# Optimization experiments

Measured on AMD Instinct MI355X. Metric: run time of the kernel, lower is better.

## Reference

```python
import jax, jax.numpy as jnp
import numpy as np

TEMPERATURE = 0.1
NUM_CLASSES = 4  # matches fill_max of labels
NEG_INF = -1e9
EPS = 1e-6


def setup_inputs() -> dict:
    key = jax.random.key(0)
    k1, k2 = jax.random.split(key)
    emb = jax.random.normal(k1, (2, 128, 64, 64), dtype=jnp.float32)
    labels = jax.random.randint(k2, (2, 64, 64), 0, NUM_CLASSES, dtype=jnp.int32)
    return {"emb": emb, "labels": labels}


def reference(emb, labels):
    B, C, H, W = emb.shape
    e = emb.transpose(0, 2, 3, 1).reshape(B * H * W, C)      # [N, C]
    lab = labels.reshape(B * H * W)                           # [N]
    # F.normalize(dim=1) with eps clamp
    norm = jnp.maximum(jnp.linalg.norm(e, axis=1, keepdims=True), 1e-12)
    e = e / norm
    n = e.shape[0]
    logits = (e @ e.T) / TEMPERATURE                          # [N, N]
    diag = jnp.arange(n)
    logits = logits.at[diag, diag].set(NEG_INF)               # mask self
    ex = jnp.exp(logits)                                      # [N, N]
    same = lab[:, None] == lab[None, :]                       # [N, N] bool
    pos_sum = jnp.sum(jnp.where(same, ex, 0.0), axis=1)       # [N]
    tot_sum = jnp.sum(ex, axis=1)                             # [N]
    row_loss = -jnp.log(pos_sum / (tot_sum + EPS))            # [N]
    # per-class mean, averaged over classes present (== torch.unique loop)
    sums = jax.ops.segment_sum(row_loss, lab, num_segments=NUM_CLASSES)
    counts = jax.ops.segment_sum(jnp.ones_like(row_loss), lab, num_segments=NUM_CLASSES)
    present = counts > 0
    per_cls = jnp.where(present, sums / jnp.maximum(counts, 1.0), 0.0)
    return per_cls.sum() / present.sum()
```

## Files before the change

kernel.cpp:

```cpp
#include <hip/hip_runtime.h>
#include <hip/hip_bf16.h>

#define N_PIX 8192
#define C_DIM 128
#define HW 4096
#define PRESCALE 3.7982825f
#define NUM_CLASSES 4

typedef __attribute__((ext_vector_type(8))) short short8;
typedef __attribute__((ext_vector_type(4))) float float4v;


__global__ __launch_bounds__(256) void normscale_kernel(const float* __restrict__ emb,
                                                        unsigned short* __restrict__ ebfT,
                                                        float* __restrict__ pz) {
    const int tid = threadIdx.x;
    const int p16 = tid & 15;
    const int g = tid >> 4;
    const int n = blockIdx.x * 16 + p16;
    const int b = n >> 12;
    const int hw = n & (HW - 1);
    const float* base = emb + b * (C_DIM * HW) + hw;

    float v[8];
    float ss = 0.f;
#pragma unroll
    for (int i = 0; i < 8; ++i) {
        v[i] = base[(g * 8 + i) * HW];
        ss += v[i] * v[i];
    }
    ss += __shfl_xor(ss, 16, 64);
    ss += __shfl_xor(ss, 32, 64);
    __shared__ float red[4][16];
    const int wv = tid >> 6;
    if ((tid & 63) < 16) red[wv][p16] = ss;
    __syncthreads();
    float tot = red[0][p16] + red[1][p16] + red[2][p16] + red[3][p16];
    float inv = PRESCALE / fmaxf(sqrtf(tot), 1e-12f);

    unsigned short us[8];
#pragma unroll
    for (int i = 0; i < 8; ++i) {
        __hip_bfloat16 h = __float2bfloat16(v[i] * inv);
        us[i] = *reinterpret_cast<unsigned short*>(&h);
    }
    const int s = g >> 2, quad = g & 3;
    unsigned short* dst = ebfT + (((blockIdx.x * 4 + s) * 64 + quad * 16 + p16) << 3);
    *reinterpret_cast<short8*>(dst) = *reinterpret_cast<short8*>(us);

    if (blockIdx.x < 64) pz[blockIdx.x * 256 + tid] = 0.f;
}

__global__ __launch_bounds__(256, 4) void pairwise_kernel(const unsigned short* __restrict__ ebfT,
                                                          const int* __restrict__ lab,
                                                          float* __restrict__ pos,
                                                          float* __restrict__ tot) {
    const int bi = blockIdx.x;
    const int d = blockIdx.y + 1;
    if (d == 32 && bi >= 32) return;
    const bool diag = (d == 33);
    const int jp = diag ? bi : ((bi + d) & 63);
    const int Ipanel = bi << 7;
    const int Jpanel = jp << 7;

    const int wave = threadIdx.x >> 6;
    const int lane = threadIdx.x & 63;
    const int quad = lane >> 4;
    const int lq = lane & 15;

    const int I0 = Ipanel + wave * 32;

    __shared__ float2 cpart[4][8][64];

    short8 afrag[2][4];
#pragma unroll
    for (int a = 0; a < 2; ++a) {
        const unsigned short* ab = ebfT + ((((I0 >> 4) + a) * 4) * 64 + lane) * 8;
#pragma unroll
        for (int s = 0; s < 4; ++s)
            afrag[a][s] = *reinterpret_cast<const short8*>(ab + s * 512);
    }
    int lab_row[2][4];
#pragma unroll
    for (int a = 0; a < 2; ++a)
#pragma unroll
        for (int r = 0; r < 4; ++r) lab_row[a][r] = lab[I0 + a * 16 + quad * 4 + r];

    float tacc[2][4] = {};
    float pacc[2][4] = {};

    if (!diag) {
        const unsigned short* bbase = ebfT + ((Jpanel >> 4) * 4 * 64 + lane) * 8;
#pragma unroll 2
        for (int t = 0; t < 8; ++t) {
            const int lab_col = lab[Jpanel + t * 16 + lq];
            const unsigned short* bt = bbase + t * 2048;
            short8 bfrag[4];
#pragma unroll
            for (int s = 0; s < 4; ++s)
                bfrag[s] = *reinterpret_cast<const short8*>(bt + s * 512);

            float4v acc0 = {0.f, 0.f, 0.f, 0.f};
            float4v acc1 = {0.f, 0.f, 0.f, 0.f};
#pragma unroll
            for (int s = 0; s < 4; ++s) {
                acc0 = __builtin_amdgcn_mfma_f32_16x16x32_bf16(afrag[0][s], bfrag[s], acc0, 0, 0, 0);
                acc1 = __builtin_amdgcn_mfma_f32_16x16x32_bf16(afrag[1][s], bfrag[s], acc1, 0, 0, 0);
            }

            float colTs = 0.f, colPs = 0.f;
#pragma unroll
            for (int r = 0; r < 4; ++r) {
                float ex = __builtin_amdgcn_exp2f(acc0[r]);
                tacc[0][r] += ex;
                float pxe = (lab_row[0][r] == lab_col) ? ex : 0.f;
                pacc[0][r] += pxe;
                colTs += ex;
                colPs += pxe;
            }
#pragma unroll
            for (int r = 0; r < 4; ++r) {
                float ex = __builtin_amdgcn_exp2f(acc1[r]);
                tacc[1][r] += ex;
                float pxe = (lab_row[1][r] == lab_col) ? ex : 0.f;
                pacc[1][r] += pxe;
                colTs += ex;
                colPs += pxe;
            }
            cpart[wave][t][lane] = make_float2(colTs, colPs);
        }
    } else {
#define EPILOGUE(A, ACC, MASKED)                                            \
    {                                                                       \
        _Pragma("unroll") for (int r = 0; r < 4; ++r) {                     \
            float ex = __builtin_amdgcn_exp2f(ACC[r]);                      \
            if (MASKED) ex = (lq == quad * 4 + r) ? 0.f : ex;               \
            tacc[A][r] += ex;                                               \
            pacc[A][r] += (lab_row[A][r] == lab_col) ? ex : 0.f;            \
        }                                                                   \
    }
        const unsigned short* bbase = ebfT + ((Ipanel >> 4) * 4 * 64 + lane) * 8;
#pragma unroll 2
        for (int t = 0; t < 8; ++t) {
            const int J = Ipanel + t * 16;
            const int lab_col = lab[J + lq];
            const unsigned short* bt = bbase + t * 2048;
            short8 bfrag[4];
#pragma unroll
            for (int s = 0; s < 4; ++s)
                bfrag[s] = *reinterpret_cast<const short8*>(bt + s * 512);

            float4v acc0 = {0.f, 0.f, 0.f, 0.f};
            float4v acc1 = {0.f, 0.f, 0.f, 0.f};
#pragma unroll
            for (int s = 0; s < 4; ++s) {
                acc0 = __builtin_amdgcn_mfma_f32_16x16x32_bf16(afrag[0][s], bfrag[s], acc0, 0, 0, 0);
                acc1 = __builtin_amdgcn_mfma_f32_16x16x32_bf16(afrag[1][s], bfrag[s], acc1, 0, 0, 0);
            }
            if (J == I0) EPILOGUE(0, acc0, true) else EPILOGUE(0, acc0, false);
            if (J == I0 + 16) EPILOGUE(1, acc1, true) else EPILOGUE(1, acc1, false);
        }
#undef EPILOGUE
    }

#pragma unroll
    for (int a = 0; a < 2; ++a) {
#pragma unroll
        for (int r = 0; r < 4; ++r) {
            float t = tacc[a][r], p = pacc[a][r];
#pragma unroll
            for (int off = 1; off < 16; off <<= 1) {
                t += __shfl_xor(t, off, 64);
                p += __shfl_xor(p, off, 64);
            }
            if (lq == 0) {
                const int row = I0 + a * 16 + quad * 4 + r;
                atomicAdd(&tot[row], t);
                atomicAdd(&pos[row], p);
            }
        }
    }

    if (!diag) {
        __syncthreads();
        if (threadIdx.x < 128) {
            const int j = threadIdx.x;
            const int tt = j >> 4, jl = j & 15;
            float st = 0.f, sp = 0.f;
#pragma unroll
            for (int w = 0; w < 4; ++w)
#pragma unroll
                for (int q = 0; q < 4; ++q) {
                    float2 v = cpart[w][tt][q * 16 + jl];
                    st += v.x;
                    sp += v.y;
                }
            atomicAdd(&tot[Jpanel + j], st);
            atomicAdd(&pos[Jpanel + j], sp);
        }
    }
}

__global__ __launch_bounds__(1024) void finalize_kernel(const float* __restrict__ pos,
                                                        const float* __restrict__ tot,
                                                        const int* __restrict__ lab,
                                                        float* __restrict__ out) {
    const int tid = threadIdx.x;
    float tv[8], pv[8];
    int cl[8];
#pragma unroll
    for (int it = 0; it < 8; ++it) {
        const int n = it * 1024 + tid;
        tv[it] = tot[n];
        pv[it] = pos[n];
        cl[it] = lab[n];
    }
    float ls[NUM_CLASSES] = {0.f, 0.f, 0.f, 0.f};
    float lc[NUM_CLASSES] = {0.f, 0.f, 0.f, 0.f};
#pragma unroll
    for (int it = 0; it < 8; ++it) {
        float rl = logf(tv[it] + 1e-6f) - logf(pv[it]);
#pragma unroll
        for (int k = 0; k < NUM_CLASSES; ++k) {
            if (cl[it] == k) {
                ls[k] += rl;
                lc[k] += 1.f;
            }
        }
    }
#pragma unroll
    for (int off = 1; off < 64; off <<= 1) {
#pragma unroll
        for (int k = 0; k < NUM_CLASSES; ++k) {
            ls[k] += __shfl_xor(ls[k], off, 64);
            lc[k] += __shfl_xor(lc[k], off, 64);
        }
    }
    __shared__ float ssum[16][NUM_CLASSES];
    __shared__ float scnt[16][NUM_CLASSES];
    const int wid = tid >> 6;
    if ((tid & 63) == 0) {
#pragma unroll
        for (int k = 0; k < NUM_CLASSES; ++k) {
            ssum[wid][k] = ls[k];
            scnt[wid][k] = lc[k];
        }
    }
    __syncthreads();
    if (tid == 0) {
        float acc = 0.f;
        int present = 0;
        for (int k = 0; k < NUM_CLASSES; ++k) {
            float s = 0.f, c = 0.f;
            for (int w = 0; w < 16; ++w) {
                s += ssum[w][k];
                c += scnt[w][k];
            }
            if (c > 0.f) {
                acc += s / c;
                present++;
            }
        }
        out[0] = acc / (float)(present > 0 ? present : 1);
    }
}

extern "C" void kernel_launch(void* const* d_in, const int* in_sizes, int n_in,
                              void* d_out, int out_size, void* d_ws, size_t ws_size,
                              hipStream_t stream) {
    const float* emb = (const float*)d_in[0];
    const int* lab = (const int*)d_in[1];
    float* out = (float*)d_out;

    unsigned short* ebfT = (unsigned short*)d_ws;
    float* pos = (float*)((char*)d_ws + N_PIX * C_DIM * 2);
    float* tot = pos + N_PIX;

    normscale_kernel<<<N_PIX / 16, 256, 0, stream>>>(emb, ebfT, pos);

    dim3 grid(64, 33);
    pairwise_kernel<<<grid, 256, 0, stream>>>(ebfT, lab, pos, tot);

    finalize_kernel<<<1, 1024, 0, stream>>>(pos, tot, lab, out);
}
```

Before: 88.56 us.

## Replace per-row float atomics with slot-partitioned partial sums and parallel reduce

The pairwise kernel now writes its per-row and per-column partial exp sums into dedicated slots indexed by diagonal offset, instead of doing atomicAdd into shared row accumulators. A new 64-block reduce kernel sums the 64 slots per row, computes row losses, and accumulates per-class sums with atomics. The last block to finish, detected through a counter, writes the final scalar. This removes atomic contention and replaces the single-block finalize. The cost is about 4 MB of extra partial-sum traffic and a slot-mapping scheme that must cover each row exactly once.

```diff
diff --git a/kernel.cpp b/kernel.cpp
--- a/kernel.cpp
+++ b/kernel.cpp
@@ -6,6 +6,7 @@
 #define HW 4096
 #define PRESCALE 3.7982825f
 #define NUM_CLASSES 4
+#define NSLOT 65
 
 typedef __attribute__((ext_vector_type(8))) short short8;
 typedef __attribute__((ext_vector_type(4))) float float4v;
@@ -13,7 +14,7 @@
 
 __global__ __launch_bounds__(256) void normscale_kernel(const float* __restrict__ emb,
                                                         unsigned short* __restrict__ ebfT,
-                                                        float* __restrict__ pz) {
+                                                        unsigned* __restrict__ czero) {
     const int tid = threadIdx.x;
     const int p16 = tid & 15;
     const int g = tid >> 4;
@@ -48,13 +49,13 @@
     unsigned short* dst = ebfT + (((blockIdx.x * 4 + s) * 64 + quad * 16 + p16) << 3);
     *reinterpret_cast<short8*>(dst) = *reinterpret_cast<short8*>(us);
 
-    if (blockIdx.x < 64) pz[blockIdx.x * 256 + tid] = 0.f;
+    if (blockIdx.x == 0 && tid < 9) czero[tid] = 0u;
 }
 
 __global__ __launch_bounds__(256, 4) void pairwise_kernel(const unsigned short* __restrict__ ebfT,
                                                           const int* __restrict__ lab,
-                                                          float* __restrict__ pos,
-                                                          float* __restrict__ tot) {
+                                                          float* __restrict__ tpart,
+                                                          float* __restrict__ ppart) {
     const int bi = blockIdx.x;
     const int d = blockIdx.y + 1;
     if (d == 32 && bi >= 32) return;
@@ -163,20 +164,24 @@
 #undef EPILOGUE
     }
 
-#pragma unroll
-    for (int a = 0; a < 2; ++a) {
-#pragma unroll
-        for (int r = 0; r < 4; ++r) {
-            float t = tacc[a][r], p = pacc[a][r];
-#pragma unroll
-            for (int off = 1; off < 16; off <<= 1) {
-                t += __shfl_xor(t, off, 64);
-                p += __shfl_xor(p, off, 64);
-            }
-            if (lq == 0) {
-                const int row = I0 + a * 16 + quad * 4 + r;
-                atomicAdd(&tot[row], t);
-                atomicAdd(&pos[row], p);
+    {
+        float* trow = tpart + (d - 1) * N_PIX;
+        float* prow = ppart + (d - 1) * N_PIX;
+#pragma unroll
+        for (int a = 0; a < 2; ++a) {
+#pragma unroll
+            for (int r = 0; r < 4; ++r) {
+                float t = tacc[a][r], p = pacc[a][r];
+#pragma unroll
+                for (int off = 1; off < 16; off <<= 1) {
+                    t += __shfl_xor(t, off, 64);
+                    p += __shfl_xor(p, off, 64);
+                }
+                if (lq == 0) {
+                    const int row = I0 + a * 16 + quad * 4 + r;
+                    trow[row] = t;
+                    prow[row] = p;
+                }
             }
         }
     }
@@ -195,38 +200,39 @@
                     st += v.x;
                     sp += v.y;
                 }
-            atomicAdd(&tot[Jpanel + j], st);
-            atomicAdd(&pos[Jpanel + j], sp);
+            tpart[(32 + d) * N_PIX + Jpanel + j] = st;
+            ppart[(32 + d) * N_PIX + Jpanel + j] = sp;
         }
     }
 }
 
-__global__ __launch_bounds__(1024) void finalize_kernel(const float* __restrict__ pos,
-                                                        const float* __restrict__ tot,
-                                                        const int* __restrict__ lab,
-                                                        float* __restrict__ out) {
+__global__ __launch_bounds__(128) void reduce_kernel(const float* __restrict__ tpart,
+                                                     const float* __restrict__ ppart,
+                                                     const int* __restrict__ lab,
+                                                     float* __restrict__ csum,
+                                                     float* __restrict__ ccnt,
+                                                     unsigned* __restrict__ cnt,
+                                                     float* __restrict__ out) {
+    const int bi = blockIdx.x;
     const int tid = threadIdx.x;
-    float tv[8], pv[8];
-    int cl[8];
-#pragma unroll
-    for (int it = 0; it < 8; ++it) {
-        const int n = it * 1024 + tid;
-        tv[it] = tot[n];
-        pv[it] = pos[n];
-        cl[it] = lab[n];
-    }
-    float ls[NUM_CLASSES] = {0.f, 0.f, 0.f, 0.f};
-    float lc[NUM_CLASSES] = {0.f, 0.f, 0.f, 0.f};
-#pragma unroll
-    for (int it = 0; it < 8; ++it) {
-        float rl = logf(tv[it] + 1e-6f) - logf(pv[it]);
-#pragma unroll
-        for (int k = 0; k < NUM_CLASSES; ++k) {
-            if (cl[it] == k) {
-                ls[k] += rl;
-                lc[k] += 1.f;
-            }
-        }
+    const int row = bi * 128 + tid;
+    const bool lowhalf = (bi < 32);
+
+    float ts = 0.f, ps = 0.f;
+#pragma unroll 8
+    for (int s = 0; s < 64; ++s) {
+        const int slot = (s == 31) ? (lowhalf ? 31 : 64) : s;
+        ts += tpart[slot * N_PIX + row];
+        ps += ppart[slot * N_PIX + row];
+    }
+    const float rl = logf(ts + 1e-6f) - logf(ps);
+    const int c = lab[row];
+
+    float ls[NUM_CLASSES], lc[NUM_CLASSES];
+#pragma unroll
+    for (int k = 0; k < NUM_CLASSES; ++k) {
+        ls[k] = (c == k) ? rl : 0.f;
+        lc[k] = (c == k) ? 1.f : 0.f;
     }
 #pragma unroll
     for (int off = 1; off < 64; off <<= 1) {
@@ -236,8 +242,8 @@
             lc[k] += __shfl_xor(lc[k], off, 64);
         }
     }
-    __shared__ float ssum[16][NUM_CLASSES];
-    __shared__ float scnt[16][NUM_CLASSES];
+    __shared__ float ssum[2][NUM_CLASSES];
+    __shared__ float scnt[2][NUM_CLASSES];
     const int wid = tid >> 6;
     if ((tid & 63) == 0) {
 #pragma unroll
@@ -247,17 +253,29 @@
         }
     }
     __syncthreads();
+    if (tid == 0) {
+#pragma unroll
+        for (int k = 0; k < NUM_CLASSES; ++k) {
+            atomicAdd(&csum[k], ssum[0][k] + ssum[1][k]);
+            atomicAdd(&ccnt[k], scnt[0][k] + scnt[1][k]);
+        }
+    }
+
+    __shared__ unsigned slast;
+    if (tid == 0)
+        slast = (__hip_atomic_fetch_add(cnt, 1u, __ATOMIC_ACQ_REL, __HIP_MEMORY_SCOPE_AGENT) == 63u)
+                    ? 1u : 0u;
+    __syncthreads();
+    if (slast == 0u) return;
+
     if (tid == 0) {
         float acc = 0.f;
         int present = 0;
         for (int k = 0; k < NUM_CLASSES; ++k) {
-            float s = 0.f, c = 0.f;
-            for (int w = 0; w < 16; ++w) {
-                s += ssum[w][k];
-                c += scnt[w][k];
-            }
-            if (c > 0.f) {
-                acc += s / c;
+            float s = __hip_atomic_load(&csum[k], __ATOMIC_RELAXED, __HIP_MEMORY_SCOPE_AGENT);
+            float c2 = __hip_atomic_load(&ccnt[k], __ATOMIC_RELAXED, __HIP_MEMORY_SCOPE_AGENT);
+            if (c2 > 0.f) {
+                acc += s / c2;
                 present++;
             }
         }
@@ -273,13 +291,16 @@
     float* out = (float*)d_out;
 
     unsigned short* ebfT = (unsigned short*)d_ws;
-    float* pos = (float*)((char*)d_ws + N_PIX * C_DIM * 2);
-    float* tot = pos + N_PIX;
-
-    normscale_kernel<<<N_PIX / 16, 256, 0, stream>>>(emb, ebfT, pos);
+    float* tpart = (float*)((char*)d_ws + N_PIX * C_DIM * 2);
+    float* ppart = tpart + NSLOT * N_PIX;
+    float* csum = ppart + NSLOT * N_PIX;
+    float* ccnt = csum + NUM_CLASSES;
+    unsigned* cnt = (unsigned*)(ccnt + NUM_CLASSES);
+
+    normscale_kernel<<<N_PIX / 16, 256, 0, stream>>>(emb, ebfT, (unsigned*)csum);
 
     dim3 grid(64, 33);
-    pairwise_kernel<<<grid, 256, 0, stream>>>(ebfT, lab, pos, tot);
-
-    finalize_kernel<<<1, 1024, 0, stream>>>(pos, tot, lab, out);
+    pairwise_kernel<<<grid, 256, 0, stream>>>(ebfT, lab, tpart, ppart);
+
+    reduce_kernel<<<64, 128, 0, stream>>>(tpart, ppart, lab, csum, ccnt, cnt, out);
 }
```

Result: slower. 94.59 us (+6.8%).
